# Kernel optimization log

Hardware: AMD Instinct MI355X
Metric: run time of the kernel (lower is better)

The kernel has to match this reference:

```python
import jax, jax.numpy as jnp
import numpy as np

NUM_USERS = 100000
NUM_BOOKS = 50000
HIDDEN = 128
USER_FEAT = 256
BOOK_FEAT = 256
E_PER_REL = 500000
NUM_LAYERS = 2


def setup_inputs() -> dict:
    key = jax.random.key(0)
    ks = jax.random.split(key, 10)
    user_x = jax.random.normal(ks[0], (NUM_USERS, USER_FEAT), dtype=jnp.float32)
    book_x = jax.random.normal(ks[1], (NUM_BOOKS, BOOK_FEAT), dtype=jnp.float32)
    user_W = jax.random.normal(ks[2], (HIDDEN, USER_FEAT), dtype=jnp.float32) * 0.05
    user_b = jax.random.normal(ks[3], (HIDDEN,), dtype=jnp.float32) * 0.05
    book_W = jax.random.normal(ks[4], (HIDDEN, BOOK_FEAT), dtype=jnp.float32) * 0.05
    book_b = jax.random.normal(ks[5], (HIDDEN,), dtype=jnp.float32) * 0.05
    # edge_index[0] = user indices, edge_index[1] = book indices
    rates_edge = jnp.stack([
        jax.random.randint(ks[6], (E_PER_REL,), 0, NUM_USERS),
        jax.random.randint(ks[7], (E_PER_REL,), 0, NUM_BOOKS)])
    implicit_edge = jnp.stack([
        jax.random.randint(ks[8], (E_PER_REL,), 0, NUM_USERS),
        jax.random.randint(ks[9], (E_PER_REL,), 0, NUM_BOOKS)])
    return {"user_x": user_x, "book_x": book_x, "user_W": user_W,
            "user_b": user_b, "book_W": book_W, "book_b": book_b,
            "rates_edge": rates_edge, "implicit_edge": implicit_edge}


def _lightgcn(user_x, book_x, user_W, user_b, book_W, book_b, rates_edge, implicit_edge):
    num_users = user_x.shape[0]
    num_nodes = num_users + book_x.shape[0]
    # input projections
    cu = user_x @ user_W.T + user_b  # [U, H]
    cb = book_x @ book_W.T + book_b  # [B, H]
    user_embeds = [cu]
    book_embeds = [cb]
    # build full directed edge list exactly as in the torch source
    all_edges = jnp.concatenate([rates_edge, implicit_edge], axis=1)  # [2, E]
    book_to_user = jnp.stack([all_edges[1] + num_users, all_edges[0]])
    full_edge = jnp.concatenate([all_edges, book_to_user], axis=1)  # [2, 2E]
    row, col = full_edge[0], full_edge[1]
    # symmetric degree normalization (edges fixed across layers)
    deg = jax.ops.segment_sum(jnp.ones(col.shape, dtype=cu.dtype), col,
                              num_segments=num_nodes)
    deg_inv_sqrt = jnp.where(deg > 0, jax.lax.rsqrt(jnp.maximum(deg, 1.0) * 0 + jnp.where(deg > 0, deg, 1.0)), 0.0)
    deg_inv_sqrt = jnp.where(deg > 0, jax.lax.rsqrt(jnp.where(deg > 0, deg, 1.0)), 0.0)
    norm = deg_inv_sqrt[row] * deg_inv_sqrt[col]  # [2E]
    for _ in range(NUM_LAYERS):
        x = jnp.concatenate([cu, cb], axis=0)  # [U+B, H]
        msg = x[row] * norm[:, None]           # gather + scale, [2E, H]
        out = jax.ops.segment_sum(msg, col, num_segments=num_nodes)  # scatter-add
        cu = out[:num_users]
        cb = out[num_users:]
        user_embeds.append(cu)
        book_embeds.append(cb)
    final_user = jnp.mean(jnp.stack(user_embeds), axis=0)
    final_book = jnp.mean(jnp.stack(book_embeds), axis=0)
    return final_user, final_book


def reference(user_x, book_x, user_W, user_b, book_W, book_b, rates_edge, implicit_edge):
    return _lightgcn(user_x, book_x, user_W, user_b, book_W, book_b,
                     rates_edge, implicit_edge)
```

## Files before the change

kernel.cpp:

```cpp
#include <hip/hip_runtime.h>

#define NUSERS 100000
#define NBOOKS 50000
#define HID 128
#define FEAT 256
#define EPR 500000
#define NEDGE (2 * EPR)

#define UBLK ((NUSERS + 127) / 128)
#define BBLK ((NBOOKS + 127) / 128)
#define GEMM_BLOCKS (UBLK + BBLK)
#define HIST_BLOCKS ((NEDGE + 1023) / 1024)
#define FILL_B ((NEDGE + 255) / 256)
#define DIS_B ((NUSERS + 255) / 256)

typedef __attribute__((ext_vector_type(8))) short bf16x8;
typedef __attribute__((ext_vector_type(4))) float f32x4;

__device__ __forceinline__ unsigned short f2bf(float f) {
  union { float f; unsigned u; } v; v.f = f;
  unsigned r = v.u + 0x7FFFu + ((v.u >> 16) & 1u);
  return (unsigned short)(r >> 16);
}
__device__ __forceinline__ float bf2f(unsigned short h) {
  union { unsigned u; float f; } v; v.u = ((unsigned)h) << 16;
  return v.f;
}

__global__ void cast_w(const float* __restrict__ w0, const float* __restrict__ w1,
                       unsigned short* __restrict__ o0, unsigned short* __restrict__ o1)
{
  int i = blockIdx.x * 256 + threadIdx.x;
  if (i < HID * FEAT) { o0[i] = f2bf(w0[i]); o1[i] = f2bf(w1[i]); }
}

__device__ __forceinline__ void decode_edge(const int* __restrict__ rates,
                                            const int* __restrict__ impl,
                                            int i, int& u, int& bk)
{
  if (i < EPR) { u = rates[i]; bk = rates[EPR + i]; }
  else { int j = i - EPR; u = impl[j]; bk = impl[EPR + j]; }
}

__global__ __launch_bounds__(256) void gemm_hist(
    const float* __restrict__ Xu, const float* __restrict__ Xb,
    const unsigned short* __restrict__ Wu, const unsigned short* __restrict__ Wb,
    const float* __restrict__ bu, const float* __restrict__ bb,
    unsigned short* __restrict__ cu0b, float* __restrict__ outb,
    float* __restrict__ outu,
    const int* __restrict__ rates, const int* __restrict__ impl,
    int* __restrict__ degu, int* __restrict__ cntb,
    unsigned int* __restrict__ relpos)
{
  __shared__ unsigned short Asb[128 * 128];
  const int bid = blockIdx.x;
  const int tid = threadIdx.x;

  int gid;
  if (bid < 2 * HIST_BLOCKS) {
    if (bid & 1) {
      const int hb = bid >> 1;
#pragma unroll
      for (int q = 0; q < 4; ++q) {
        int i = hb * 1024 + q * 256 + tid;
        if (i < NEDGE) {
          int u, bk;
          decode_edge(rates, impl, i, u, bk);
          relpos[i] = (unsigned int)atomicAdd(&cntb[bk], 1);
          atomicAdd(&degu[u], 1);
        }
      }
      return;
    }
    gid = bid >> 1;
  } else {
    gid = bid - HIST_BLOCKS;
  }

  const bool isU = gid < UBLK;
  const float* __restrict__ X = isU ? Xu : Xb;
  const unsigned short* __restrict__ W = isU ? Wu : Wb;
  const float* __restrict__ bias = isU ? bu : bb;
  const int M  = isU ? NUSERS : NBOOKS;
  const int bm = (isU ? gid : gid - UBLK) * 128;

  const int lane = tid & 63;
  const int wv   = tid >> 6;
  const int l15  = lane & 15, l4 = lane >> 4;
  const int row0 = wv * 32;

  f32x4 acc[2][8];
#pragma unroll
  for (int mi = 0; mi < 2; ++mi)
#pragma unroll
    for (int ni = 0; ni < 8; ++ni) acc[mi][ni] = (f32x4)0.f;

#pragma unroll
  for (int h = 0; h < 2; ++h) {
    if (h) __syncthreads();

#pragma unroll
    for (int c8 = 0; c8 < 2; ++c8) {
      float4 tmp[8];
#pragma unroll
      for (int k = 0; k < 8; ++k) {
        int o = (c8 * 8 + k) * 256 + tid;
        int row = o >> 5, c4 = o & 31;
        int gr = bm + row; if (gr > M - 1) gr = M - 1;
        tmp[k] = *reinterpret_cast<const float4*>(&X[(size_t)gr * FEAT + h * 128 + c4 * 4]);
      }
#pragma unroll
      for (int k = 0; k < 8; ++k) {
        int o = (c8 * 8 + k) * 256 + tid;
        int row = o >> 5, c4 = o & 31;
        int slot = (c4 >> 1) ^ (row & 15);
        ushort4 w4;
        w4.x = f2bf(tmp[k].x); w4.y = f2bf(tmp[k].y);
        w4.z = f2bf(tmp[k].z); w4.w = f2bf(tmp[k].w);
        *reinterpret_cast<ushort4*>(
            reinterpret_cast<char*>(Asb) + row * 256 + slot * 16 + (c4 & 1) * 8) = w4;
      }
    }
    __syncthreads();

#pragma unroll
    for (int ks = 0; ks < 4; ++ks) {
      const int kg = h * 4 + ks;
      bf16x8 bfr[8];
#pragma unroll
      for (int ni = 0; ni < 8; ++ni) {
        int col = ni * 16 + l15;
        bfr[ni] = *reinterpret_cast<const bf16x8*>(&W[(size_t)col * FEAT + kg * 32 + l4 * 8]);
      }
      bf16x8 a[2];
#pragma unroll
      for (int mi = 0; mi < 2; ++mi) {
        int rt = row0 + mi * 16 + l15;
        int slot = (ks * 4 + l4) ^ l15;
        a[mi] = *reinterpret_cast<const bf16x8*>(
            reinterpret_cast<const char*>(Asb) + rt * 256 + slot * 16);
      }
#pragma unroll
      for (int ni = 0; ni < 8; ++ni) {
        acc[0][ni] = __builtin_amdgcn_mfma_f32_16x16x32_bf16(a[0], bfr[ni], acc[0][ni], 0, 0, 0);
        acc[1][ni] = __builtin_amdgcn_mfma_f32_16x16x32_bf16(a[1], bfr[ni], acc[1][ni], 0, 0, 0);
      }
    }
  }

#pragma unroll
  for (int ni = 0; ni < 8; ++ni) {
    int col = ni * 16 + l15;
    float bj = bias[col];
#pragma unroll
    for (int mi = 0; mi < 2; ++mi) {
#pragma unroll
      for (int j = 0; j < 4; ++j) {
        int rr = bm + row0 + mi * 16 + l4 * 4 + j;
        if (rr < M) {
          float vv = acc[mi][ni][j] + bj;
          if (isU) {
            cu0b[(size_t)rr * HID + col] = f2bf(vv);
            if (rr >= NBOOKS) outu[(size_t)rr * HID + col] = vv * (1.0f / 3.0f);
          } else {
            outb[(size_t)rr * HID + col] = vv * (1.0f / 3.0f);
          }
        }
      }
    }
  }
}

__global__ void fill_dis(const int* __restrict__ rates, const int* __restrict__ impl,
                         const int* __restrict__ offs,
                         const unsigned int* __restrict__ relpos,
                         int* __restrict__ brow,
                         const int* __restrict__ degu, const int* __restrict__ cntb,
                         float* __restrict__ dis)
{
  int b = blockIdx.x;
  if (b >= FILL_B) {
    int i = (b - FILL_B) * 256 + threadIdx.x;
    if (i < NUSERS) {
      int d = degu[i] + (i < NBOOKS ? cntb[i] : 0);
      dis[i] = (d > 0) ? rsqrtf((float)d) : 0.f;
    }
    return;
  }
  int i = b * 256 + threadIdx.x;
  if (i >= NEDGE) return;
  int u, bk;
  decode_edge(rates, impl, i, u, bk);
  brow[offs[bk] + (int)relpos[i]] = u;
}

__global__ __launch_bounds__(1024) void scan_blocks(const int* __restrict__ counts,
                                                    int* __restrict__ offs,
                                                    int* __restrict__ bsum, int N)
{
  __shared__ int buf[1024];
  int t = threadIdx.x;
  int i = blockIdx.x * 1024 + t;
  int v = (i < N) ? counts[i] : 0;
  buf[t] = v;
  __syncthreads();
  for (int off = 1; off < 1024; off <<= 1) {
    int x = (t >= off) ? buf[t - off] : 0;
    __syncthreads();
    buf[t] += x;
    __syncthreads();
  }
  int incl = buf[t];
  if (i < N) offs[i] = incl - v;
  if (t == 1023) bsum[blockIdx.x] = incl;
}

__global__ void scan_totals(const int* __restrict__ bsum, int* __restrict__ bpre,
                            int* __restrict__ offs, int nb, int N)
{
  if (threadIdx.x == 0 && blockIdx.x == 0) {
    int run = 0;
    for (int b = 0; b < nb; ++b) { bpre[b] = run; run += bsum[b]; }
    offs[N] = run;
  }
}

__global__ void add_prefix(int* __restrict__ offs, const int* __restrict__ bpre, int N)
{
  int i = blockIdx.x * blockDim.x + threadIdx.x;
  if (i < N) offs[i] += bpre[i >> 10];
}

__global__ __launch_bounds__(256) void pull1(const unsigned short* __restrict__ srcb,
    const int* __restrict__ offs, const int* __restrict__ brow,
    const float* __restrict__ dis, unsigned short* __restrict__ dstb)
{
  int c = (blockIdx.x << 2) + (threadIdx.x >> 6);
  if (c >= NBOOKS) return;
  const int lane = threadIdx.x & 63;
  const int g = lane >> 4, l = lane & 15;
  const int s = offs[c], e = offs[c + 1];

  float acc[8];
#pragma unroll
  for (int j = 0; j < 8; ++j) acc[j] = 0.f;

  int i = s + g;
  for (; i + 4 < e; i += 8) {
    int rr0 = brow[i], rr1 = brow[i + 4];
    float w0 = dis[rr0], w1 = dis[rr1];
    bf16x8 v0 = *reinterpret_cast<const bf16x8*>(&srcb[(size_t)rr0 * HID + l * 8]);
    bf16x8 v1 = *reinterpret_cast<const bf16x8*>(&srcb[(size_t)rr1 * HID + l * 8]);
#pragma unroll
    for (int j = 0; j < 8; ++j) acc[j] += w0 * bf2f((unsigned short)v0[j]);
#pragma unroll
    for (int j = 0; j < 8; ++j) acc[j] += w1 * bf2f((unsigned short)v1[j]);
  }
  if (i < e) {
    int rr = brow[i];
    float w = dis[rr];
    bf16x8 v = *reinterpret_cast<const bf16x8*>(&srcb[(size_t)rr * HID + l * 8]);
#pragma unroll
    for (int j = 0; j < 8; ++j) acc[j] += w * bf2f((unsigned short)v[j]);
  }

#pragma unroll
  for (int j = 0; j < 8; ++j) {
    acc[j] += __shfl_xor(acc[j], 16, 64);
    acc[j] += __shfl_xor(acc[j], 32, 64);
  }
  if (g == 0) {
    float db = dis[c];
    bf16x8 o;
#pragma unroll
    for (int j = 0; j < 8; ++j) o[j] = (short)f2bf(db * acc[j]);
    *reinterpret_cast<bf16x8*>(&dstb[(size_t)c * HID + l * 8]) = o;
  }
}

__global__ __launch_bounds__(256) void pull2_final(const unsigned short* __restrict__ h1b,
    const int* __restrict__ offs, const int* __restrict__ brow,
    const float* __restrict__ dis, const unsigned short* __restrict__ cu0b,
    float* __restrict__ outu)
{
  int c = (blockIdx.x << 2) + (threadIdx.x >> 6);
  if (c >= NBOOKS) return;
  const int lane = threadIdx.x & 63;
  const int g = lane >> 4, l = lane & 15;
  const int s = offs[c], e = offs[c + 1];

  float acc[8];
#pragma unroll
  for (int j = 0; j < 8; ++j) acc[j] = 0.f;

  int i = s + g;
  for (; i + 4 < e; i += 8) {
    int rr0 = brow[i], rr1 = brow[i + 4];
    int rc0 = rr0 < NBOOKS ? rr0 : 0;
    int rc1 = rr1 < NBOOKS ? rr1 : 0;
    float w0 = rr0 < NBOOKS ? dis[rr0] : 0.f;
    float w1 = rr1 < NBOOKS ? dis[rr1] : 0.f;
    bf16x8 v0 = *reinterpret_cast<const bf16x8*>(&h1b[(size_t)rc0 * HID + l * 8]);
    bf16x8 v1 = *reinterpret_cast<const bf16x8*>(&h1b[(size_t)rc1 * HID + l * 8]);
#pragma unroll
    for (int j = 0; j < 8; ++j) acc[j] += w0 * bf2f((unsigned short)v0[j]);
#pragma unroll
    for (int j = 0; j < 8; ++j) acc[j] += w1 * bf2f((unsigned short)v1[j]);
  }
  if (i < e) {
    int rr = brow[i];
    int rc = rr < NBOOKS ? rr : 0;
    float w = rr < NBOOKS ? dis[rr] : 0.f;
    bf16x8 v = *reinterpret_cast<const bf16x8*>(&h1b[(size_t)rc * HID + l * 8]);
#pragma unroll
    for (int j = 0; j < 8; ++j) acc[j] += w * bf2f((unsigned short)v[j]);
  }

#pragma unroll
  for (int j = 0; j < 8; ++j) {
    acc[j] += __shfl_xor(acc[j], 16, 64);
    acc[j] += __shfl_xor(acc[j], 32, 64);
  }
  if (g == 0) {
    float db = dis[c];
    size_t idx = (size_t)c * HID + l * 8;
    bf16x8 c0 = *reinterpret_cast<const bf16x8*>(&cu0b[idx]);
    bf16x8 h1 = *reinterpret_cast<const bf16x8*>(&h1b[idx]);
    float r[8];
#pragma unroll
    for (int j = 0; j < 8; ++j)
      r[j] = (bf2f((unsigned short)c0[j]) + bf2f((unsigned short)h1[j]) + db * acc[j]) * (1.0f / 3.0f);
    *reinterpret_cast<float4*>(&outu[idx])     = make_float4(r[0], r[1], r[2], r[3]);
    *reinterpret_cast<float4*>(&outu[idx + 4]) = make_float4(r[4], r[5], r[6], r[7]);
  }
}

extern "C" void kernel_launch(void* const* d_in, const int* in_sizes, int n_in,
                              void* d_out, int out_size, void* d_ws, size_t ws_size,
                              hipStream_t stream)
{
  const float* user_x = (const float*)d_in[0];
  const float* book_x = (const float*)d_in[1];
  const float* user_W = (const float*)d_in[2];
  const float* user_b = (const float*)d_in[3];
  const float* book_W = (const float*)d_in[4];
  const float* book_b = (const float*)d_in[5];
  const int*   rates  = (const int*)d_in[6];
  const int*   impl   = (const int*)d_in[7];

  float* out      = (float*)d_out;
  float* out_user = out;
  float* out_book = out + (size_t)NUSERS * HID;

  char* p = (char*)d_ws;
  auto carve = [&](size_t bytes) -> void* {
    void* r = (void*)p;
    p += (bytes + 255) & ~(size_t)255;
    return r;
  };
  unsigned short* cu0b   = (unsigned short*)carve((size_t)NUSERS * HID * 2);
  unsigned short* h1b    = (unsigned short*)carve((size_t)NBOOKS * HID * 2);
  unsigned short* wub    = (unsigned short*)carve((size_t)HID * FEAT * 2);
  unsigned short* wbb    = (unsigned short*)carve((size_t)HID * FEAT * 2);
  int*          degu   = (int*)carve((size_t)NUSERS * 4);
  int*          cntb   = (int*)carve((size_t)NBOOKS * 4);
  float*        dis    = (float*)carve((size_t)NUSERS * 4);
  int*          offs   = (int*)carve((size_t)(NBOOKS + 2) * 4);
  int*          bsum   = (int*)carve(256 * 4);
  int*          bpre   = (int*)carve(256 * 4);
  unsigned int* relpos = (unsigned int*)carve((size_t)NEDGE * 4);
  int*          brow   = (int*)carve((size_t)NEDGE * 4);

  hipMemsetAsync(degu, 0, (size_t)NUSERS * 4, stream);
  hipMemsetAsync(cntb, 0, (size_t)NBOOKS * 4, stream);

  cast_w<<<(HID * FEAT + 255) / 256, 256, 0, stream>>>(user_W, book_W, wub, wbb);

  gemm_hist<<<GEMM_BLOCKS + HIST_BLOCKS, 256, 0, stream>>>(
      user_x, book_x, wub, wbb, user_b, book_b,
      cu0b, out_book, out_user, rates, impl, degu, cntb, relpos);

  const int nb = (NBOOKS + 1023) / 1024;
  scan_blocks<<<nb, 1024, 0, stream>>>(cntb, offs, bsum, NBOOKS);
  scan_totals<<<1, 64, 0, stream>>>(bsum, bpre, offs, nb, NBOOKS);
  add_prefix<<<(NBOOKS + 255) / 256, 256, 0, stream>>>(offs, bpre, NBOOKS);

  fill_dis<<<FILL_B + DIS_B, 256, 0, stream>>>(rates, impl, offs, relpos, brow,
                                               degu, cntb, dis);

  pull1<<<(NBOOKS + 3) / 4, 256, 0, stream>>>(cu0b, offs, brow, dis, h1b);
  pull2_final<<<(NBOOKS + 3) / 4, 256, 0, stream>>>(h1b, offs, brow, dis, cu0b, out_user);
}
```

Baseline: 271.4 us.

## Fuse histogram into every GEMM block and stream fp32 tiles via direct LDS loads

```diff
diff --git a/kernel.cpp b/kernel.cpp
--- a/kernel.cpp
+++ b/kernel.cpp
@@ -7,10 +7,9 @@
 #define EPR 500000
 #define NEDGE (2 * EPR)
 
-#define UBLK ((NUSERS + 127) / 128)
-#define BBLK ((NBOOKS + 127) / 128)
-#define GEMM_BLOCKS (UBLK + BBLK)
-#define HIST_BLOCKS ((NEDGE + 1023) / 1024)
+#define UBLK64 ((NUSERS + 63) / 64)
+#define BBLK64 ((NBOOKS + 63) / 64)
+#define GH_BLOCKS (UBLK64 + BBLK64)
 #define FILL_B ((NEDGE + 255) / 256)
 #define DIS_B ((NUSERS + 255) / 256)
 
@@ -25,6 +24,11 @@
 __device__ __forceinline__ float bf2f(unsigned short h) {
   union { unsigned u; float f; } v; v.u = ((unsigned)h) << 16;
   return v.f;
+}
+__device__ __forceinline__ unsigned pk2bf(float lo, float hi) {
+  unsigned r;
+  asm("v_cvt_pk_bf16_f32 %0, %1, %2" : "=v"(r) : "v"(lo), "v"(hi));
+  return r;
 }
 
 __global__ void cast_w(const float* __restrict__ w0, const float* __restrict__ w1,
@@ -50,102 +54,79 @@
     float* __restrict__ outu,
     const int* __restrict__ rates, const int* __restrict__ impl,
     int* __restrict__ degu, int* __restrict__ cntb,
-    unsigned int* __restrict__ relpos)
-{
-  __shared__ unsigned short Asb[128 * 128];
+    int* __restrict__ relpos)
+{
+  __shared__ float Asb[64 * 256];
   const int bid = blockIdx.x;
   const int tid = threadIdx.x;
 
-  int gid;
-  if (bid < 2 * HIST_BLOCKS) {
-    if (bid & 1) {
-      const int hb = bid >> 1;
-#pragma unroll
-      for (int q = 0; q < 4; ++q) {
-        int i = hb * 1024 + q * 256 + tid;
-        if (i < NEDGE) {
-          int u, bk;
-          decode_edge(rates, impl, i, u, bk);
-          relpos[i] = (unsigned int)atomicAdd(&cntb[bk], 1);
-          atomicAdd(&degu[u], 1);
-        }
-      }
-      return;
-    }
-    gid = bid >> 1;
-  } else {
-    gid = bid - HIST_BLOCKS;
-  }
-
-  const bool isU = gid < UBLK;
+  const int e0 = bid * 512 + tid;
+  const int e1 = e0 + 256;
+  const bool v0 = e0 < NEDGE, v1 = e1 < NEDGE;
+  int p0 = 0, p1 = 0;
+  if (v0) {
+    int u, bk;
+    decode_edge(rates, impl, e0, u, bk);
+    p0 = atomicAdd(&cntb[bk], 1);
+    atomicAdd(&degu[u], 1);
+  }
+  if (v1) {
+    int u, bk;
+    decode_edge(rates, impl, e1, u, bk);
+    p1 = atomicAdd(&cntb[bk], 1);
+    atomicAdd(&degu[u], 1);
+  }
+
+  const bool isU = bid < UBLK64;
   const float* __restrict__ X = isU ? Xu : Xb;
   const unsigned short* __restrict__ W = isU ? Wu : Wb;
   const float* __restrict__ bias = isU ? bu : bb;
   const int M  = isU ? NUSERS : NBOOKS;
-  const int bm = (isU ? gid : gid - UBLK) * 128;
+  const int bm = (isU ? bid : bid - UBLK64) * 64;
 
   const int lane = tid & 63;
   const int wv   = tid >> 6;
   const int l15  = lane & 15, l4 = lane >> 4;
-  const int row0 = wv * 32;
-
-  f32x4 acc[2][8];
-#pragma unroll
-  for (int mi = 0; mi < 2; ++mi)
-#pragma unroll
-    for (int ni = 0; ni < 8; ++ni) acc[mi][ni] = (f32x4)0.f;
-
-#pragma unroll
-  for (int h = 0; h < 2; ++h) {
-    if (h) __syncthreads();
-
-#pragma unroll
-    for (int c8 = 0; c8 < 2; ++c8) {
-      float4 tmp[8];
-#pragma unroll
-      for (int k = 0; k < 8; ++k) {
-        int o = (c8 * 8 + k) * 256 + tid;
-        int row = o >> 5, c4 = o & 31;
-        int gr = bm + row; if (gr > M - 1) gr = M - 1;
-        tmp[k] = *reinterpret_cast<const float4*>(&X[(size_t)gr * FEAT + h * 128 + c4 * 4]);
-      }
-#pragma unroll
-      for (int k = 0; k < 8; ++k) {
-        int o = (c8 * 8 + k) * 256 + tid;
-        int row = o >> 5, c4 = o & 31;
-        int slot = (c4 >> 1) ^ (row & 15);
-        ushort4 w4;
-        w4.x = f2bf(tmp[k].x); w4.y = f2bf(tmp[k].y);
-        w4.z = f2bf(tmp[k].z); w4.w = f2bf(tmp[k].w);
-        *reinterpret_cast<ushort4*>(
-            reinterpret_cast<char*>(Asb) + row * 256 + slot * 16 + (c4 & 1) * 8) = w4;
-      }
-    }
-    __syncthreads();
-
-#pragma unroll
-    for (int ks = 0; ks < 4; ++ks) {
-      const int kg = h * 4 + ks;
-      bf16x8 bfr[8];
-#pragma unroll
-      for (int ni = 0; ni < 8; ++ni) {
-        int col = ni * 16 + l15;
-        bfr[ni] = *reinterpret_cast<const bf16x8*>(&W[(size_t)col * FEAT + kg * 32 + l4 * 8]);
-      }
-      bf16x8 a[2];
-#pragma unroll
-      for (int mi = 0; mi < 2; ++mi) {
-        int rt = row0 + mi * 16 + l15;
-        int slot = (ks * 4 + l4) ^ l15;
-        a[mi] = *reinterpret_cast<const bf16x8*>(
-            reinterpret_cast<const char*>(Asb) + rt * 256 + slot * 16);
-      }
-#pragma unroll
-      for (int ni = 0; ni < 8; ++ni) {
-        acc[0][ni] = __builtin_amdgcn_mfma_f32_16x16x32_bf16(a[0], bfr[ni], acc[0][ni], 0, 0, 0);
-        acc[1][ni] = __builtin_amdgcn_mfma_f32_16x16x32_bf16(a[1], bfr[ni], acc[1][ni], 0, 0, 0);
-      }
-    }
+
+#pragma unroll
+  for (int rnd = 0; rnd < 16; ++rnd) {
+    int o   = wv * 1024 + rnd * 64 + lane;
+    int row = o >> 6;
+    int pc  = o & 63;
+    int lc  = pc ^ (row & 7);
+    int gr  = bm + row; if (gr > M - 1) gr = M - 1;
+    __builtin_amdgcn_global_load_lds(
+        (const float*)&X[(size_t)gr * FEAT + lc * 4],
+        &Asb[(size_t)(wv * 1024 + rnd * 64) * 4], 16, 0, 0);
+  }
+  __syncthreads();
+
+  f32x4 acc[8];
+#pragma unroll
+  for (int ni = 0; ni < 8; ++ni) acc[ni] = (f32x4)0.f;
+
+  const int arow = wv * 16 + l15;
+  const int m7   = l15 & 7;
+#pragma unroll
+  for (int ks = 0; ks < 8; ++ks) {
+    bf16x8 bfr[8];
+#pragma unroll
+    for (int ni = 0; ni < 8; ++ni)
+      bfr[ni] = *reinterpret_cast<const bf16x8*>(
+          &W[(size_t)(ni * 16 + l15) * FEAT + ks * 32 + l4 * 8]);
+
+    int lc0 = ks * 8 + l4 * 2;
+    f32x4 a0 = *reinterpret_cast<const f32x4*>(&Asb[arow * 256 + ((lc0    ) ^ m7) * 4]);
+    f32x4 a1 = *reinterpret_cast<const f32x4*>(&Asb[arow * 256 + ((lc0 + 1) ^ m7) * 4]);
+    union { unsigned u32[4]; bf16x8 v; } au;
+    au.u32[0] = pk2bf(a0[0], a0[1]);
+    au.u32[1] = pk2bf(a0[2], a0[3]);
+    au.u32[2] = pk2bf(a1[0], a1[1]);
+    au.u32[3] = pk2bf(a1[2], a1[3]);
+
+#pragma unroll
+    for (int ni = 0; ni < 8; ++ni)
+      acc[ni] = __builtin_amdgcn_mfma_f32_16x16x32_bf16(au.v, bfr[ni], acc[ni], 0, 0, 0);
   }
 
 #pragma unroll
@@ -153,27 +134,27 @@
     int col = ni * 16 + l15;
     float bj = bias[col];
 #pragma unroll
-    for (int mi = 0; mi < 2; ++mi) {
-#pragma unroll
-      for (int j = 0; j < 4; ++j) {
-        int rr = bm + row0 + mi * 16 + l4 * 4 + j;
-        if (rr < M) {
-          float vv = acc[mi][ni][j] + bj;
-          if (isU) {
-            cu0b[(size_t)rr * HID + col] = f2bf(vv);
-            if (rr >= NBOOKS) outu[(size_t)rr * HID + col] = vv * (1.0f / 3.0f);
-          } else {
-            outb[(size_t)rr * HID + col] = vv * (1.0f / 3.0f);
-          }
+    for (int j = 0; j < 4; ++j) {
+      int rr = bm + wv * 16 + l4 * 4 + j;
+      if (rr < M) {
+        float vv = acc[ni][j] + bj;
+        if (isU) {
+          cu0b[(size_t)rr * HID + col] = f2bf(vv);
+          if (rr >= NBOOKS) outu[(size_t)rr * HID + col] = vv * (1.0f / 3.0f);
+        } else {
+          outb[(size_t)rr * HID + col] = vv * (1.0f / 3.0f);
         }
       }
     }
   }
+
+  if (v0) relpos[e0] = p0;
+  if (v1) relpos[e1] = p1;
 }
 
 __global__ void fill_dis(const int* __restrict__ rates, const int* __restrict__ impl,
                          const int* __restrict__ offs,
-                         const unsigned int* __restrict__ relpos,
+                         const int* __restrict__ relpos,
                          int* __restrict__ brow,
                          const int* __restrict__ degu, const int* __restrict__ cntb,
                          float* __restrict__ dis)
@@ -191,7 +172,7 @@
   if (i >= NEDGE) return;
   int u, bk;
   decode_edge(rates, impl, i, u, bk);
-  brow[offs[bk] + (int)relpos[i]] = u;
+  brow[offs[bk] + relpos[i]] = u;
 }
 
 __global__ __launch_bounds__(1024) void scan_blocks(const int* __restrict__ counts,
@@ -362,21 +343,21 @@
   unsigned short* h1b    = (unsigned short*)carve((size_t)NBOOKS * HID * 2);
   unsigned short* wub    = (unsigned short*)carve((size_t)HID * FEAT * 2);
   unsigned short* wbb    = (unsigned short*)carve((size_t)HID * FEAT * 2);
-  int*          degu   = (int*)carve((size_t)NUSERS * 4);
-  int*          cntb   = (int*)carve((size_t)NBOOKS * 4);
-  float*        dis    = (float*)carve((size_t)NUSERS * 4);
-  int*          offs   = (int*)carve((size_t)(NBOOKS + 2) * 4);
-  int*          bsum   = (int*)carve(256 * 4);
-  int*          bpre   = (int*)carve(256 * 4);
-  unsigned int* relpos = (unsigned int*)carve((size_t)NEDGE * 4);
-  int*          brow   = (int*)carve((size_t)NEDGE * 4);
+  int*   degu   = (int*)carve((size_t)NUSERS * 4);
+  int*   cntb   = (int*)carve((size_t)NBOOKS * 4);
+  float* dis    = (float*)carve((size_t)NUSERS * 4);
+  int*   offs   = (int*)carve((size_t)(NBOOKS + 2) * 4);
+  int*   bsum   = (int*)carve(256 * 4);
+  int*   bpre   = (int*)carve(256 * 4);
+  int*   relpos = (int*)carve((size_t)NEDGE * 4);
+  int*   brow   = (int*)carve((size_t)NEDGE * 4);
 
   hipMemsetAsync(degu, 0, (size_t)NUSERS * 4, stream);
   hipMemsetAsync(cntb, 0, (size_t)NBOOKS * 4, stream);
 
   cast_w<<<(HID * FEAT + 255) / 256, 256, 0, stream>>>(user_W, book_W, wub, wbb);
 
-  gemm_hist<<<GEMM_BLOCKS + HIST_BLOCKS, 256, 0, stream>>>(
+  gemm_hist<<<GH_BLOCKS, 256, 0, stream>>>(
       user_x, book_x, wub, wbb, user_b, book_b,
       cu0b, out_book, out_user, rates, impl, degu, cntb, relpos);
 
```

After: 278.5 us. 2.6% more time.
